# Optimization experiments

Hardware: AMD Instinct MI355X
Metric: run time of the kernel (lower is better)

The kernel has to match this reference:

```python
import jax, jax.numpy as jnp
import numpy as np

N_NODES = 100000


def gcn_conv(x, edge_index, W, b):
    """GCNConv: out = D^-1/2 (A + I) D^-1/2 (x W) + b, with added self-loops."""
    n = x.shape[0]
    xw = x @ W  # [N, C]
    loop = jnp.arange(n, dtype=edge_index.dtype)
    src = jnp.concatenate([edge_index[0], loop])  # [E+N]
    dst = jnp.concatenate([edge_index[1], loop])
    deg = jax.ops.segment_sum(jnp.ones_like(dst, dtype=xw.dtype), dst, num_segments=n)
    dinv = jax.lax.rsqrt(jnp.where(deg > 0, deg, 1.0))
    norm = dinv[src] * dinv[dst]  # [E+N]
    msgs = xw[src] * norm[:, None]  # gather + scale
    out = jax.ops.segment_sum(msgs, dst, num_segments=n)  # scatter-add
    return out + b


def setup_inputs() -> dict:
    key = jax.random.key(0)
    k1, k2, k3, k4, k5 = jax.random.split(key, 5)
    F_in, C1, C2 = 256, 64, 40
    E = 3200000
    x = jax.random.normal(k1, (N_NODES, F_in), dtype=jnp.float32)
    edge_index = jax.random.randint(k2, (2, E), 0, N_NODES, dtype=jnp.int64)
    W1 = jax.random.normal(k3, (F_in, C1), dtype=jnp.float32) / np.sqrt(F_in)
    b1 = jnp.zeros((C1,), dtype=jnp.float32)
    W2 = jax.random.normal(k4, (C1, C2), dtype=jnp.float32) / np.sqrt(C1)
    b2 = jnp.zeros((C2,), dtype=jnp.float32)
    return {"x": x, "edge_index": edge_index, "W1": W1, "b1": b1, "W2": W2, "b2": b2}


def reference(x, edge_index, W1, b1, W2, b2):
    h1 = jax.nn.relu(gcn_conv(x, edge_index, W1, b1))
    # dropout is identity in eval mode (training=False)
    h2 = gcn_conv(h1, edge_index, W2, b2)
    return jax.nn.log_softmax(h2, axis=1)
```

## Files before the change

### kernel.cpp

```cpp
#include <hip/hip_runtime.h>
#include <math.h>

#define NN 100000
#define NB 256
#define RANGE 392
#define CAP 56
#define BCAP 13824
#define NBLK_PART 512

typedef unsigned int uint;
typedef __attribute__((ext_vector_type(8))) short short8;
typedef __attribute__((ext_vector_type(4))) float f32x4;
typedef __attribute__((ext_vector_type(2))) float f32x2;


__global__ __launch_bounds__(256) void partition_kernel(const int* __restrict__ src,
                                                        const int* __restrict__ dst,
                                                        int* __restrict__ bcur,
                                                        unsigned* __restrict__ bkt, int E) {
    __shared__ unsigned stage[NB * CAP];
    __shared__ int lcnt[NB];
    __shared__ int baseS[NB];
    for (int i = threadIdx.x; i < NB; i += 256) lcnt[i] = 0;
    __syncthreads();

    const int nq = E >> 2;
    const int stride = gridDim.x * blockDim.x;
    for (int q = blockIdx.x * blockDim.x + threadIdx.x; q < nq; q += stride) {
        const int4 s4 = ((const int4*)src)[q];
        const int4 d4 = ((const int4*)dst)[q];
#pragma unroll
        for (int k = 0; k < 4; k++) {
            const int s = (&s4.x)[k];
            const int d = (&d4.x)[k];
            const unsigned b = (unsigned)d / RANGE;
            const unsigned ent = ((unsigned)s << 9) | ((unsigned)d - b * RANGE);
            const int slot = atomicAdd(&lcnt[b], 1);
            if (slot < CAP) {
                stage[b * CAP + slot] = ent;
            } else {
                const int pos = atomicAdd(&bcur[b], 1);
                if (pos < BCAP) bkt[(size_t)b * BCAP + pos] = ent;
            }
        }
    }
    const int gid = blockIdx.x * blockDim.x + threadIdx.x;
    if (gid < (E & 3)) {
        const int e = (E & ~3) + gid;
        const int s = src[e], d = dst[e];
        const unsigned b = (unsigned)d / RANGE;
        const unsigned ent = ((unsigned)s << 9) | ((unsigned)d - b * RANGE);
        const int pos = atomicAdd(&bcur[b], 1);
        if (pos < BCAP) bkt[(size_t)b * BCAP + pos] = ent;
    }
    __syncthreads();

    if (threadIdx.x < NB) {
        const int c = min(lcnt[threadIdx.x], CAP);
        baseS[threadIdx.x] = (c > 0) ? atomicAdd(&bcur[threadIdx.x], c) : 0;
    }
    __syncthreads();

    const int w = threadIdx.x >> 6, l = threadIdx.x & 63;
    for (int b = w; b < NB; b += 4) {
        const int cnt = min(lcnt[b], CAP);
        const int base = baseS[b];
        for (int i = l; i < cnt; i += 64) {
            const int pos = base + i;
            if (pos < BCAP) bkt[(size_t)b * BCAP + pos] = stage[b * CAP + i];
        }
    }
}


__global__ __launch_bounds__(256) void bucket_sort_kernel(const int* __restrict__ bcur,
                                                          unsigned* __restrict__ bkt,
                                                          int* __restrict__ row_off,
                                                          int* __restrict__ deg,
                                                          float* __restrict__ dinv, int n) {
    __shared__ int sortedS[BCAP];
    __shared__ int cntS[RANGE];
    __shared__ int offS[RANGE];
    const int b = blockIdx.x;
    const int tid = threadIdx.x;
    unsigned* eb = bkt + (size_t)b * BCAP;
    const int m = min(bcur[b], BCAP);

    for (int i = tid; i < RANGE; i += 256) cntS[i] = 0;
    __syncthreads();
    for (int i = tid; i < m; i += 256) atomicAdd(&cntS[(int)(eb[i] & 511u)], 1);
    __syncthreads();

    if (tid < 64) {
        const int l = tid;
        int carry = 0;
        for (int base = 0; base < RANGE; base += 64) {
            const int i = base + l;
            const int c = (i < RANGE) ? cntS[i] : 0;
            int v = c;
#pragma unroll
            for (int off = 1; off < 64; off <<= 1) {
                const int t2 = __shfl_up(v, off);
                if (l >= off) v += t2;
            }
            if (i < RANGE) offS[i] = carry + v - c;
            carry += __shfl(v, 63);
        }
    }
    __syncthreads();

    for (int i = tid; i < RANGE; i += 256) {
        const int node = b * RANGE + i;
        if (node < n) {
            row_off[node] = b * BCAP + offS[i];
            deg[node] = cntS[i];
            dinv[node] = rsqrtf((float)cntS[i] + 1.0f);
        }
    }
    __syncthreads();

    for (int i = tid; i < m; i += 256) {
        const unsigned e = eb[i];
        const int pos = atomicAdd(&offS[(int)(e & 511u)], 1);
        sortedS[pos] = (int)(e >> 9);
    }
    __syncthreads();

    for (int i = tid; i < m; i += 256) eb[i] = (unsigned)sortedS[i];
}

__device__ inline uint pack_bf16(float a, float b) {
    uint ua = __float_as_uint(a), ub = __float_as_uint(b);
    ua = (ua + 0x7fffu + ((ua >> 16) & 1u)) >> 16;
    ub = (ub + 0x7fffu + ((ub >> 16) & 1u)) & 0xffff0000u;
    return ua | ub;
}
__device__ inline unsigned short bf16r(float f) {
    uint u = __float_as_uint(f);
    return (unsigned short)((u + 0x7fffu + ((u >> 16) & 1u)) >> 16);
}
__device__ inline void acc_bf16x8p(f32x2* acc, uint4 v) {
    const uint u[4] = {v.x, v.y, v.z, v.w};
#pragma unroll
    for (int i = 0; i < 4; i++) {
        f32x2 t;
        t.x = __uint_as_float(u[i] << 16);
        t.y = __uint_as_float(u[i] & 0xffff0000u);
        acc[i] += t;
    }
}


template <int K, int CREAL>
__global__ __launch_bounds__(256) void gemm_mfma_kernel(const float* __restrict__ x,
                                                        const float* __restrict__ W,
                                                        const float* __restrict__ dinv,
                                                        unsigned short* __restrict__ y,
                                                        int n) {
    constexpr int KP = K + 8;
    __shared__ unsigned short wt[64 * KP];
    __shared__ unsigned short as[128 * 40];
    const int t = threadIdx.x;
    const int l = t & 63;
    const int w = t >> 6;
    const int lane15 = l & 15;
    const int quad = l >> 4;
    const int row0 = blockIdx.x * 128;

    if (blockIdx.x == 0 && t < 64) y[(size_t)n * 64 + t] = 0;

    for (int idx = t; idx < K * 16; idx += 256) {
        const int k = idx >> 4;
        const int c4 = (idx & 15) * 4;
        float4 g = make_float4(0.f, 0.f, 0.f, 0.f);
        if (c4 < CREAL) g = *(const float4*)(W + (size_t)k * CREAL + c4);
        wt[(c4 + 0) * KP + k] = bf16r(g.x);
        wt[(c4 + 1) * KP + k] = bf16r(g.y);
        wt[(c4 + 2) * KP + k] = bf16r(g.z);
        wt[(c4 + 3) * KP + k] = bf16r(g.w);
    }

    f32x4 acc[2][4];
#pragma unroll
    for (int mt = 0; mt < 2; mt++)
#pragma unroll
        for (int nt = 0; nt < 4; nt++) acc[mt][nt] = (f32x4){0.f, 0.f, 0.f, 0.f};

    float4 g[4];
#pragma unroll
    for (int p = 0; p < 4; p++) {
        const int idx = t + p * 256;
        const int row = idx >> 3;
        const int kq = idx & 7;
        const int gr = min(row0 + row, n - 1);
        g[p] = *(const float4*)(x + (size_t)gr * K + kq * 4);
    }

    for (int kc = 0; kc < K; kc += 32) {
        __syncthreads();
#pragma unroll
        for (int p = 0; p < 4; p++) {
            const int idx = t + p * 256;
            const int row = idx >> 3;
            const int kq = idx & 7;
            uint2 pk;
            pk.x = pack_bf16(g[p].x, g[p].y);
            pk.y = pack_bf16(g[p].z, g[p].w);
            *(uint2*)(as + row * 40 + kq * 4) = pk;
        }
        if (kc + 32 < K) {
#pragma unroll
            for (int p = 0; p < 4; p++) {
                const int idx = t + p * 256;
                const int row = idx >> 3;
                const int kq = idx & 7;
                const int gr = min(row0 + row, n - 1);
                g[p] = *(const float4*)(x + (size_t)gr * K + kc + 32 + kq * 4);
            }
        }
        __syncthreads();

        short8 bf[4];
#pragma unroll
        for (int nt = 0; nt < 4; nt++)
            bf[nt] = *(const short8*)(wt + (nt * 16 + lane15) * KP + kc + quad * 8);
#pragma unroll
        for (int mt = 0; mt < 2; mt++) {
            const short8 af =
                *(const short8*)(as + (w * 32 + mt * 16 + lane15) * 40 + quad * 8);
#pragma unroll
            for (int nt = 0; nt < 4; nt++)
                acc[mt][nt] =
                    __builtin_amdgcn_mfma_f32_16x16x32_bf16(af, bf[nt], acc[mt][nt], 0, 0, 0);
        }
    }

#pragma unroll
    for (int mt = 0; mt < 2; mt++) {
#pragma unroll
        for (int r = 0; r < 4; r++) {
            const int row = row0 + w * 32 + mt * 16 + quad * 4 + r;
            if (row < n) {
                const float di = dinv[row];
#pragma unroll
                for (int nt = 0; nt < 4; nt++)
                    y[(size_t)row * 64 + nt * 16 + lane15] = bf16r(acc[mt][nt][r] * di);
            }
        }
    }
}


__global__ __launch_bounds__(256) void agg64_kernel(const unsigned short* __restrict__ y,
                                                    const int* __restrict__ row_off,
                                                    const int* __restrict__ deg,
                                                    const unsigned* __restrict__ nbr,
                                                    const float* __restrict__ dinv,
                                                    const float* __restrict__ b,
                                                    float* __restrict__ out, int n) {
    int node = blockIdx.x * 4 + (threadIdx.x >> 6);
    if (node >= n) return;
    const int l = threadIdx.x & 63;
    const int g = l >> 3;
    const int cq = l & 7;

    const int start = row_off[node];
    const int dg = deg[node];

    const uint4 vself = ((const uint4*)(y + (size_t)node * 64))[cq];

    f32x2 acc[4];
#pragma unroll
    for (int i = 0; i < 4; i++) acc[i] = (f32x2){0.f, 0.f};

    for (int base = 0; base < dg; base += 64) {
        const int m = min(64, dg - base);
        const int idx = (l < m) ? (int)nbr[start + base + l] : n;
        uint4 v[8];
#pragma unroll
        for (int j = 0; j < 8; j++)
            if (j * 8 < m) {
                const int s = __shfl(idx, j * 8 + g);
                v[j] = ((const uint4*)(y + (size_t)s * 64))[cq];
            }
#pragma unroll
        for (int j = 0; j < 8; j++)
            if (j * 8 < m) acc_bf16x8p(acc, v[j]);
    }
#pragma unroll
    for (int off = 8; off < 64; off <<= 1)
#pragma unroll
        for (int i = 0; i < 4; i++) {
            f32x2 t;
            t.x = __shfl_xor(acc[i].x, off);
            t.y = __shfl_xor(acc[i].y, off);
            acc[i] += t;
        }

    f32x2 self[4];
#pragma unroll
    for (int i = 0; i < 4; i++) self[i] = (f32x2){0.f, 0.f};
    acc_bf16x8p(self, vself);
    const float* af = (const float*)acc;
    const float* sf = (const float*)self;
    const float di = dinv[node];
    const float4 bv0 = *(const float4*)(b + cq * 8);
    const float4 bv1 = *(const float4*)(b + cq * 8 + 4);
    const float bb[8] = {bv0.x, bv0.y, bv0.z, bv0.w, bv1.x, bv1.y, bv1.z, bv1.w};
    if (l < 8) {
        float4 o0, o1;
        o0.x = fmaxf((af[0] + sf[0]) * di + bb[0], 0.f);
        o0.y = fmaxf((af[1] + sf[1]) * di + bb[1], 0.f);
        o0.z = fmaxf((af[2] + sf[2]) * di + bb[2], 0.f);
        o0.w = fmaxf((af[3] + sf[3]) * di + bb[3], 0.f);
        o1.x = fmaxf((af[4] + sf[4]) * di + bb[4], 0.f);
        o1.y = fmaxf((af[5] + sf[5]) * di + bb[5], 0.f);
        o1.z = fmaxf((af[6] + sf[6]) * di + bb[6], 0.f);
        o1.w = fmaxf((af[7] + sf[7]) * di + bb[7], 0.f);
        *(float4*)(out + (size_t)node * 64 + l * 8) = o0;
        *(float4*)(out + (size_t)node * 64 + l * 8 + 4) = o1;
    }
}


__global__ __launch_bounds__(256) void agg40_lsm_kernel(const unsigned short* __restrict__ y,
                                                        const int* __restrict__ row_off,
                                                        const int* __restrict__ deg,
                                                        const unsigned* __restrict__ nbr,
                                                        const float* __restrict__ dinv,
                                                        const float* __restrict__ b,
                                                        float* __restrict__ out, int n) {
    int node = blockIdx.x * 4 + (threadIdx.x >> 6);
    if (node >= n) return;
    const int l = threadIdx.x & 63;
    int gg = l / 5;
    int cq = l - gg * 5;
    if (l >= 60) { gg = 11; cq = l - 60; }

    const int start = row_off[node];
    const int dg = deg[node];

    const uint4 vself = *((const uint4*)(y + (size_t)node * 64) + cq);

    f32x2 acc[4];
#pragma unroll
    for (int i = 0; i < 4; i++) acc[i] = (f32x2){0.f, 0.f};

    for (int base = 0; base < dg; base += 60) {
        const int m = min(60, dg - base);
        const int idx = (l < m) ? (int)nbr[start + base + l] : n;
        uint4 v[5];
#pragma unroll
        for (int r = 0; r < 5; r++)
            if (r * 12 < m) {
                const int s = __shfl(idx, r * 12 + gg);
                v[r] = *((const uint4*)(y + (size_t)s * 64) + cq);
            }
#pragma unroll
        for (int r = 0; r < 5; r++)
            if (r * 12 < m) acc_bf16x8p(acc, v[r]);
    }

    float* af = (float*)acc;
#pragma unroll
    for (int i = 0; i < 8; i++) { const float t = __shfl_down(af[i], 30); if (l < 30) af[i] += t; }
#pragma unroll
    for (int i = 0; i < 8; i++) { const float t = __shfl_down(af[i], 15); if (l < 15) af[i] += t; }
#pragma unroll
    for (int i = 0; i < 8; i++) { const float t = __shfl_down(af[i], 5);  if (l < 5)  af[i] += t; }
#pragma unroll
    for (int i = 0; i < 8; i++) { const float t = __shfl_down(af[i], 10); if (l < 5)  af[i] += t; }

    if (l < 5) acc_bf16x8p(acc, vself);

    const float di = dinv[node];
    const float4 bv0 = *(const float4*)(b + cq * 8);
    const float4 bv1 = *(const float4*)(b + cq * 8 + 4);
    const float bb[8] = {bv0.x, bv0.y, bv0.z, bv0.w, bv1.x, bv1.y, bv1.z, bv1.w};
    float h[8];
#pragma unroll
    for (int i = 0; i < 8; i++) h[i] = af[i] * di + bb[i];

    float mx = -INFINITY;
#pragma unroll
    for (int i = 0; i < 8; i++) mx = fmaxf(mx, h[i]);
    {
        const float m0 = __shfl(mx, 0), m1 = __shfl(mx, 1), m2 = __shfl(mx, 2),
                    m3 = __shfl(mx, 3), m4 = __shfl(mx, 4);
        mx = fmaxf(fmaxf(fmaxf(m0, m1), fmaxf(m2, m3)), m4);
    }
    float es = 0.f;
#pragma unroll
    for (int i = 0; i < 8; i++) es += __expf(h[i] - mx);
    {
        const float e0 = __shfl(es, 0), e1 = __shfl(es, 1), e2 = __shfl(es, 2),
                    e3 = __shfl(es, 3), e4 = __shfl(es, 4);
        es = ((e0 + e1) + (e2 + e3)) + e4;
    }
    const float ls = mx + __logf(es);

    if (l < 5) {
        float4 o0, o1;
        o0.x = h[0] - ls; o0.y = h[1] - ls; o0.z = h[2] - ls; o0.w = h[3] - ls;
        o1.x = h[4] - ls; o1.y = h[5] - ls; o1.z = h[6] - ls; o1.w = h[7] - ls;
        *(float4*)(out + (size_t)node * 40 + cq * 8) = o0;
        *(float4*)(out + (size_t)node * 40 + cq * 8 + 4) = o1;
    }
}


extern "C" void kernel_launch(void* const* d_in, const int* in_sizes, int n_in,
                              void* d_out, int out_size, void* d_ws, size_t ws_size,
                              hipStream_t stream) {
    const float* x  = (const float*)d_in[0];
    const int* edges = (const int*)d_in[1];
    const float* W1 = (const float*)d_in[2];
    const float* b1 = (const float*)d_in[3];
    const float* W2 = (const float*)d_in[4];
    const float* b2 = (const float*)d_in[5];
    float* out = (float*)d_out;

    const int n = NN;
    const int E = in_sizes[1] / 2;

    char* ws = (char*)d_ws;
    size_t off = 0;
    auto alloc = [&](size_t bytes) -> void* {
        void* p = ws + off;
        off += (bytes + 255) & ~(size_t)255;
        return p;
    };
    int*            bcur    = (int*)alloc((size_t)NB * 4);
    unsigned*       bkt     = (unsigned*)alloc((size_t)NB * BCAP * 4);
    int*            row_off = (int*)alloc((size_t)n * 4);
    int*            deg     = (int*)alloc((size_t)n * 4);
    float*          dinv    = (float*)alloc((size_t)n * 4);
    float*          h1      = (float*)alloc((size_t)n * 64 * 4);
    unsigned short* y1      = (unsigned short*)alloc((size_t)(n + 1) * 64 * 2);
    unsigned short* y2      = y1;

    const int* src = edges;
    const int* dst = edges + E;

    hipMemsetAsync(bcur, 0, (size_t)NB * 4, stream);
    partition_kernel<<<NBLK_PART, 256, 0, stream>>>(src, dst, bcur, bkt, E);
    bucket_sort_kernel<<<NB, 256, 0, stream>>>(bcur, bkt, row_off, deg, dinv, n);

    const int gblk = (n + 127) / 128;

    gemm_mfma_kernel<256, 64><<<gblk, 256, 0, stream>>>(x, W1, dinv, y1, n);
    agg64_kernel<<<(n + 3) / 4, 256, 0, stream>>>(y1, row_off, deg, bkt, dinv, b1, h1, n);

    gemm_mfma_kernel<64, 40><<<gblk, 256, 0, stream>>>(h1, W2, dinv, y2, n);
    agg40_lsm_kernel<<<(n + 3) / 4, 256, 0, stream>>>(y2, row_off, deg, bkt, dinv, b2, out, n);
}
```

Baseline: 373.0 us.

## Fuse layer-2 GEMM into layer-1 aggregation epilogue via shuffles

The layer-1 aggregation kernel now applies bias and ReLU, then multiplies each node's 64-wide hidden row by W2 (staged in shared memory) using wave shuffles, scales by dinv, and writes bf16 y2 directly. This removes the fp32 h1 round trip through global memory and one kernel launch. The cost is 64 shuffles plus LDS reads per lane for every node, a W2 load into shared memory in every block, and a separate y2 buffer. The padding row at index n of y2 is zeroed inside the kernel.

```diff
diff --git a/kernel.cpp b/kernel.cpp
--- a/kernel.cpp
+++ b/kernel.cpp
@@ -12,6 +12,7 @@
 typedef __attribute__((ext_vector_type(8))) short short8;
 typedef __attribute__((ext_vector_type(4))) float f32x4;
 typedef __attribute__((ext_vector_type(2))) float f32x2;
+typedef __attribute__((ext_vector_type(4))) uint u32x4;
 
 
 __global__ __launch_bounds__(256) void partition_kernel(const int* __restrict__ src,
@@ -251,14 +252,21 @@
 }
 
 
-__global__ __launch_bounds__(256) void agg64_kernel(const unsigned short* __restrict__ y,
-                                                    const int* __restrict__ row_off,
-                                                    const int* __restrict__ deg,
-                                                    const unsigned* __restrict__ nbr,
-                                                    const float* __restrict__ dinv,
-                                                    const float* __restrict__ b,
-                                                    float* __restrict__ out, int n) {
-    int node = blockIdx.x * 4 + (threadIdx.x >> 6);
+__global__ __launch_bounds__(256) void agg64_gemm2_kernel(const unsigned short* __restrict__ y,
+                                                          const int* __restrict__ row_off,
+                                                          const int* __restrict__ deg,
+                                                          const unsigned* __restrict__ nbr,
+                                                          const float* __restrict__ dinv,
+                                                          const float* __restrict__ b1,
+                                                          const float* __restrict__ W2,
+                                                          unsigned short* __restrict__ y2,
+                                                          int n) {
+    __shared__ float w2s[64 * 40];
+    for (int i = threadIdx.x; i < 64 * 40; i += 256) w2s[i] = W2[i];
+    if (blockIdx.x == 0 && threadIdx.x < 64) y2[(size_t)n * 64 + threadIdx.x] = 0;
+    __syncthreads();
+
+    const int node = blockIdx.x * 4 + (threadIdx.x >> 6);
     if (node >= n) return;
     const int l = threadIdx.x & 63;
     const int g = l >> 3;
@@ -304,22 +312,26 @@
     const float* af = (const float*)acc;
     const float* sf = (const float*)self;
     const float di = dinv[node];
-    const float4 bv0 = *(const float4*)(b + cq * 8);
-    const float4 bv1 = *(const float4*)(b + cq * 8 + 4);
+    const float4 bv0 = *(const float4*)(b1 + cq * 8);
+    const float4 bv1 = *(const float4*)(b1 + cq * 8 + 4);
     const float bb[8] = {bv0.x, bv0.y, bv0.z, bv0.w, bv1.x, bv1.y, bv1.z, bv1.w};
-    if (l < 8) {
-        float4 o0, o1;
-        o0.x = fmaxf((af[0] + sf[0]) * di + bb[0], 0.f);
-        o0.y = fmaxf((af[1] + sf[1]) * di + bb[1], 0.f);
-        o0.z = fmaxf((af[2] + sf[2]) * di + bb[2], 0.f);
-        o0.w = fmaxf((af[3] + sf[3]) * di + bb[3], 0.f);
-        o1.x = fmaxf((af[4] + sf[4]) * di + bb[4], 0.f);
-        o1.y = fmaxf((af[5] + sf[5]) * di + bb[5], 0.f);
-        o1.z = fmaxf((af[6] + sf[6]) * di + bb[6], 0.f);
-        o1.w = fmaxf((af[7] + sf[7]) * di + bb[7], 0.f);
-        *(float4*)(out + (size_t)node * 64 + l * 8) = o0;
-        *(float4*)(out + (size_t)node * 64 + l * 8 + 4) = o1;
-    }
+    float hreg[8];
+#pragma unroll
+    for (int i = 0; i < 8; i++) hreg[i] = fmaxf((af[i] + sf[i]) * di + bb[i], 0.f);
+
+    const int c = (l < 40) ? l : 39;
+    float v = 0.f;
+#pragma unroll
+    for (int q = 0; q < 8; q++)
+#pragma unroll
+        for (int i = 0; i < 8; i++)
+            v = fmaf(__shfl(hreg[i], q), w2s[(q * 8 + i) * 40 + c], v);
+    v *= di;
+
+    const float va = __shfl(v, (l << 1));
+    const float vb = __shfl(v, (l << 1) + 1);
+    if (l < 20)
+        *((uint*)(y2 + (size_t)node * 64) + l) = pack_bf16(va, vb);
 }
 
 
@@ -435,9 +447,8 @@
     int*            row_off = (int*)alloc((size_t)n * 4);
     int*            deg     = (int*)alloc((size_t)n * 4);
     float*          dinv    = (float*)alloc((size_t)n * 4);
-    float*          h1      = (float*)alloc((size_t)n * 64 * 4);
     unsigned short* y1      = (unsigned short*)alloc((size_t)(n + 1) * 64 * 2);
-    unsigned short* y2      = y1;
+    unsigned short* y2      = (unsigned short*)alloc((size_t)(n + 1) * 64 * 2);
 
     const int* src = edges;
     const int* dst = edges + E;
@@ -449,8 +460,6 @@
     const int gblk = (n + 127) / 128;
 
     gemm_mfma_kernel<256, 64><<<gblk, 256, 0, stream>>>(x, W1, dinv, y1, n);
-    agg64_kernel<<<(n + 3) / 4, 256, 0, stream>>>(y1, row_off, deg, bkt, dinv, b1, h1, n);
-
-    gemm_mfma_kernel<64, 40><<<gblk, 256, 0, stream>>>(h1, W2, dinv, y2, n);
+    agg64_gemm2_kernel<<<(n + 3) / 4, 256, 0, stream>>>(y1, row_off, deg, bkt, dinv, b1, W2, y2, n);
     agg40_lsm_kernel<<<(n + 3) / 4, 256, 0, stream>>>(y2, row_off, deg, bkt, dinv, b2, out, n);
 }
```

Measured after the change: 446.6 us. 19.7% more time.
